# Performance work log

Hardware: AMD Instinct MI355X
Metric: run time of the kernel (lower is better)

## Reference

```python
import jax, jax.numpy as jnp
import numpy as np


def setup_inputs() -> dict:
    key = jax.random.key(0)
    ks = jax.random.split(key, 6)
    b, t, s, qu, vu, d = 8, 64, 512, 512, 512, 512
    return {
        "query": jax.random.normal(ks[0], (b, t, qu), jnp.float32),
        "value": jax.random.normal(ks[1], (b, s, vu), jnp.float32),
        "mask": jax.random.randint(ks[2], (b, s), 0, 2).astype(bool),
        "W1_w": jax.random.normal(ks[3], (qu, d), jnp.float32) * (1.0 / np.sqrt(qu)),
        "W1_b": jnp.zeros((d,), jnp.float32),
        "W2_w": jax.random.normal(ks[4], (vu, d), jnp.float32) * (1.0 / np.sqrt(vu)),
        "W2_b": jnp.zeros((d,), jnp.float32),
        "scale": jax.random.normal(ks[5], (d,), jnp.float32) * 0.05,
    }


def reference(query, value, mask, W1_w, W1_b, W2_w, W2_b, scale):
    # Dense projections
    q = jnp.einsum('btq,qd->btd', query, W1_w) + W1_b   # [b,t,d]
    k = jnp.einsum('bsv,vd->bsd', value, W2_w) + W2_b   # [b,s,d]
    # Additive (Bahdanau) score with learned scale vector (Keras use_scale=True)
    # scores[b,t,s] = sum_d scale[d] * tanh(q[b,t,d] + k[b,s,d])
    scores = jnp.einsum('btsd,d->bts', jnp.tanh(q[:, :, None, :] + k[:, None, :, :]), scale)
    # Mask over source positions (value mask); query mask is all-ones (no-op)
    scores = jnp.where(mask[:, None, :], scores, jnp.float32(-1e9))
    attention_weights = jax.nn.softmax(scores, axis=-1)   # [b,t,s]
    context_vector = jnp.einsum('bts,bsv->btv', attention_weights, value)  # [b,t,vu]
    return context_vector, attention_weights
```

## Files before the change

kernel.cpp:

```cpp
#include <hip/hip_runtime.h>
#include <hip/hip_bf16.h>

#define B_  8
#define T_  64
#define S_  512
#define D_  512

#define QN (512 * 512)
#define KN (4096 * 512)
#define SN (B_ * T_ * S_)

#define TLOG2E 2.8853900817779268f
#define LOG2E  1.4426950408889634f

typedef __attribute__((ext_vector_type(8))) short bf16x8;
typedef __attribute__((ext_vector_type(4))) float f32x4;

__device__ __forceinline__ unsigned short f2bf(float f) {
    unsigned int u = __float_as_uint(f);
    return (unsigned short)((u + 0x7FFFu + ((u >> 16) & 1u)) >> 16);
}
__device__ __forceinline__ unsigned int pk2(float a, float b) {
    return (unsigned int)f2bf(a) | ((unsigned int)f2bf(b) << 16);
}

__global__ __launch_bounds__(256) void mfma_gemm(
    const float* __restrict__ query, const float* __restrict__ value,
    const float* __restrict__ W1, const float* __restrict__ W2,
    const float* __restrict__ b1, const float* __restrict__ b2,
    float* __restrict__ qproj, float* __restrict__ kproj)
{
    __shared__ __align__(16) unsigned short Ab[64][40];
    __shared__ __align__(16) unsigned short Bs[64][40];

    const int x = blockIdx.x;
    const float *A, *W;
    float* C;
    int tm, tn;
    bool isq;
    if (x < 512) {
        tm = (x & 7) * 8 + ((x >> 3) & 7);
        tn = x >> 6;
        A = value; W = W2; C = kproj; isq = false;
    } else {
        int r = x - 512;
        tm = r >> 3; tn = r & 7;
        A = query; W = W1; C = qproj; isq = true;
    }

    const int tid  = threadIdx.x;
    const int lane = tid & 63;
    const int wid  = tid >> 6;
    const int wm = (wid & 1) * 32, wn = (wid >> 1) * 32;
    const int fm = lane & 15, fq = lane >> 4;

    f32x4 acc00 = {0.f, 0.f, 0.f, 0.f};
    f32x4 acc01 = acc00, acc10 = acc00, acc11 = acc00;

    const int ar = tid >> 2;
    const int ac = (tid & 3) * 8;
    const float* Ag = A + (size_t)(tm * 64 + ar) * 512 + ac;
    const int c0 = (tid & 15) * 4;
    const int kp = (tid >> 4) * 2;
    const float* Wg = W + (size_t)kp * 512 + tn * 64 + c0;

    float4 av0 = *(const float4*)(Ag);
    float4 av1 = *(const float4*)(Ag + 4);
    float4 wv0 = *(const float4*)(Wg);
    float4 wv1 = *(const float4*)(Wg + 512);

    for (int k0 = 0; k0 < 512; k0 += 32) {
        __syncthreads();
        {
            uint4 pa;
            pa.x = pk2(av0.x, av0.y); pa.y = pk2(av0.z, av0.w);
            pa.z = pk2(av1.x, av1.y); pa.w = pk2(av1.z, av1.w);
            *(uint4*)&Ab[ar][ac] = pa;
            *(unsigned int*)&Bs[c0 + 0][kp] = pk2(wv0.x, wv1.x);
            *(unsigned int*)&Bs[c0 + 1][kp] = pk2(wv0.y, wv1.y);
            *(unsigned int*)&Bs[c0 + 2][kp] = pk2(wv0.z, wv1.z);
            *(unsigned int*)&Bs[c0 + 3][kp] = pk2(wv0.w, wv1.w);
        }
        __syncthreads();
        const int kn = (k0 + 32) & 511;
        av0 = *(const float4*)(Ag + kn);
        av1 = *(const float4*)(Ag + kn + 4);
        wv0 = *(const float4*)(Wg + (size_t)kn * 512);
        wv1 = *(const float4*)(Wg + (size_t)kn * 512 + 512);

        bf16x8 a0  = *(const bf16x8*)&Ab[wm + fm][fq * 8];
        bf16x8 a1  = *(const bf16x8*)&Ab[wm + 16 + fm][fq * 8];
        bf16x8 b0  = *(const bf16x8*)&Bs[wn + fm][fq * 8];
        bf16x8 b1v = *(const bf16x8*)&Bs[wn + 16 + fm][fq * 8];
        acc00 = __builtin_amdgcn_mfma_f32_16x16x32_bf16(a0, b0,  acc00, 0, 0, 0);
        acc01 = __builtin_amdgcn_mfma_f32_16x16x32_bf16(a0, b1v, acc01, 0, 0, 0);
        acc10 = __builtin_amdgcn_mfma_f32_16x16x32_bf16(a1, b0,  acc10, 0, 0, 0);
        acc11 = __builtin_amdgcn_mfma_f32_16x16x32_bf16(a1, b1v, acc11, 0, 0, 0);
    }

    const int n0 = tn * 64 + wn + fm;
    const int n1 = n0 + 16;
    float bias0 = 0.f, bias1 = 0.f;
    if (isq) {
        bias0 = b1[n0] + b2[n0];
        bias1 = b1[n1] + b2[n1];
    }
    const int m0 = tm * 64 + wm + fq * 4;
#pragma unroll
    for (int r = 0; r < 4; ++r) {
        C[(size_t)(m0 + r) * 512 + n0]      = (acc00[r] + bias0) * TLOG2E;
        C[(size_t)(m0 + r) * 512 + n1]      = (acc01[r] + bias1) * TLOG2E;
        C[(size_t)(m0 + 16 + r) * 512 + n0] = (acc10[r] + bias0) * TLOG2E;
        C[(size_t)(m0 + 16 + r) * 512 + n1] = (acc11[r] + bias1) * TLOG2E;
    }
}

__global__ __launch_bounds__(256, 4) void scores_t(
    const float* __restrict__ qproj, const float* __restrict__ kproj,
    const int*   __restrict__ mask,  const float* __restrict__ scale,
    float* __restrict__ sparts)
{
    const int blk = blockIdx.x;
    const int b  = blk & 7;
    int r = blk >> 3;
    const int dh = r & 1;
    r >>= 1;
    const int sg = r & 31;
    const int tg = r >> 5;
    const int t0 = tg * 16, s0 = sg * 16;
    const int dbase = dh * 256;

    __shared__ float kT[16][132];
    __shared__ float qT[16][132];
    __shared__ float cS[128];

    const int tid  = threadIdx.x;
    const int t_l = tid >> 4;
    const int s_l = tid & 15;
    const int m = mask[b * S_ + s0 + s_l];

    const int lrow = tid >> 5;
    const int lcol = (tid & 31) * 4;

    float p0 = 0.f, p1 = 0.f;

    for (int c = 0; c < 2; ++c) {
        const int dc = dbase + c * 128;
        const float* kp = kproj + (size_t)(b * S_ + s0) * D_ + dc;
        const float* qp = qproj + (size_t)(b * T_ + t0) * D_ + dc;
        *(float4*)&kT[lrow][lcol]     = *(const float4*)(kp + (size_t)lrow * D_ + lcol);
        *(float4*)&kT[lrow + 8][lcol] = *(const float4*)(kp + (size_t)(lrow + 8) * D_ + lcol);
        *(float4*)&qT[lrow][lcol]     = *(const float4*)(qp + (size_t)lrow * D_ + lcol);
        *(float4*)&qT[lrow + 8][lcol] = *(const float4*)(qp + (size_t)(lrow + 8) * D_ + lcol);
        if (tid < 32) {
            *(float4*)&cS[tid * 4] = *(const float4*)(scale + dc + tid * 4);
        }
        __syncthreads();

#pragma unroll 4
        for (int j = 0; j < 32; ++j) {
            float4 k4 = *(const float4*)&kT[s_l][j * 4];
            float4 q4 = *(const float4*)&qT[t_l][j * 4];
            float4 c4 = *(const float4*)&cS[j * 4];
            float e0 = __builtin_amdgcn_exp2f(q4.x + k4.x);
            float e1 = __builtin_amdgcn_exp2f(q4.y + k4.y);
            float e2 = __builtin_amdgcn_exp2f(q4.z + k4.z);
            float e3 = __builtin_amdgcn_exp2f(q4.w + k4.w);
            float r0 = __builtin_amdgcn_rcpf(e0 + 1.0f);
            float r1 = __builtin_amdgcn_rcpf(e1 + 1.0f);
            float r2 = __builtin_amdgcn_rcpf(e2 + 1.0f);
            float r3 = __builtin_amdgcn_rcpf(e3 + 1.0f);
            p0 = fmaf(c4.x, r0, p0);
            p1 = fmaf(c4.y, r1, p1);
            p0 = fmaf(c4.z, r2, p0);
            p1 = fmaf(c4.w, r3, p1);
        }
        __syncthreads();
    }

    const float p = p0 + p1;
    const float out = m ? (-2.0f * p) : -5e8f;
    sparts[(size_t)dh * SN + (size_t)(b * T_ + t0 + t_l) * S_ + s0 + s_l] = out;
}

__global__ __launch_bounds__(256) void softmax_ctx(
    const float* __restrict__ sparts, const float* __restrict__ value,
    float* __restrict__ ctx, float* __restrict__ attn)
{
    const int blk = blockIdx.x;
    const int b = blk & 7;
    int r = blk >> 3;
    const int vc = r & 3;
    const int tq = r >> 2;
    const int t0 = tq * 4;
    const size_t rbase = (size_t)(b * T_ + t0) * S_;

    const int tid  = threadIdx.x;
    const int lane = tid & 63;
    const int wid  = tid >> 6;

    __shared__ float4 wp4[S_];
    __shared__ float4 part[4][8][32];
    __shared__ float4 red4[8];

    const int sa = tid, sb = tid + 256;
    float4 xa, xb;
    xa.x = sparts[rbase + sa]          + sparts[SN + rbase + sa];
    xa.y = sparts[rbase + S_ + sa]     + sparts[SN + rbase + S_ + sa];
    xa.z = sparts[rbase + 2 * S_ + sa] + sparts[SN + rbase + 2 * S_ + sa];
    xa.w = sparts[rbase + 3 * S_ + sa] + sparts[SN + rbase + 3 * S_ + sa];
    xb.x = sparts[rbase + sb]          + sparts[SN + rbase + sb];
    xb.y = sparts[rbase + S_ + sb]     + sparts[SN + rbase + S_ + sb];
    xb.z = sparts[rbase + 2 * S_ + sb] + sparts[SN + rbase + 2 * S_ + sb];
    xb.w = sparts[rbase + 3 * S_ + sb] + sparts[SN + rbase + 3 * S_ + sb];

    float4 m4;
    m4.x = fmaxf(xa.x, xb.x); m4.y = fmaxf(xa.y, xb.y);
    m4.z = fmaxf(xa.z, xb.z); m4.w = fmaxf(xa.w, xb.w);
#pragma unroll
    for (int off = 32; off >= 1; off >>= 1) {
        m4.x = fmaxf(m4.x, __shfl_xor(m4.x, off));
        m4.y = fmaxf(m4.y, __shfl_xor(m4.y, off));
        m4.z = fmaxf(m4.z, __shfl_xor(m4.z, off));
        m4.w = fmaxf(m4.w, __shfl_xor(m4.w, off));
    }
    if (lane == 0) red4[wid] = m4;
    __syncthreads();
    {
        float4 r0 = red4[0], r1 = red4[1], r2 = red4[2], r3 = red4[3];
        m4.x = fmaxf(fmaxf(r0.x, r1.x), fmaxf(r2.x, r3.x));
        m4.y = fmaxf(fmaxf(r0.y, r1.y), fmaxf(r2.y, r3.y));
        m4.z = fmaxf(fmaxf(r0.z, r1.z), fmaxf(r2.z, r3.z));
        m4.w = fmaxf(fmaxf(r0.w, r1.w), fmaxf(r2.w, r3.w));
    }

    float4 ea, eb;
    ea.x = __builtin_amdgcn_exp2f((xa.x - m4.x) * LOG2E);
    ea.y = __builtin_amdgcn_exp2f((xa.y - m4.y) * LOG2E);
    ea.z = __builtin_amdgcn_exp2f((xa.z - m4.z) * LOG2E);
    ea.w = __builtin_amdgcn_exp2f((xa.w - m4.w) * LOG2E);
    eb.x = __builtin_amdgcn_exp2f((xb.x - m4.x) * LOG2E);
    eb.y = __builtin_amdgcn_exp2f((xb.y - m4.y) * LOG2E);
    eb.z = __builtin_amdgcn_exp2f((xb.z - m4.z) * LOG2E);
    eb.w = __builtin_amdgcn_exp2f((xb.w - m4.w) * LOG2E);

    float4 s4;
    s4.x = ea.x + eb.x; s4.y = ea.y + eb.y;
    s4.z = ea.z + eb.z; s4.w = ea.w + eb.w;
#pragma unroll
    for (int off = 32; off >= 1; off >>= 1) {
        s4.x += __shfl_xor(s4.x, off);
        s4.y += __shfl_xor(s4.y, off);
        s4.z += __shfl_xor(s4.z, off);
        s4.w += __shfl_xor(s4.w, off);
    }
    if (lane == 0) red4[4 + wid] = s4;
    __syncthreads();
    {
        float4 r0 = red4[4], r1 = red4[5], r2 = red4[6], r3 = red4[7];
        s4.x = (r0.x + r1.x) + (r2.x + r3.x);
        s4.y = (r0.y + r1.y) + (r2.y + r3.y);
        s4.z = (r0.z + r1.z) + (r2.z + r3.z);
        s4.w = (r0.w + r1.w) + (r2.w + r3.w);
    }
    float4 inv4;
    inv4.x = 1.0f / s4.x; inv4.y = 1.0f / s4.y;
    inv4.z = 1.0f / s4.z; inv4.w = 1.0f / s4.w;

    float4 wa, wb;
    wa.x = ea.x * inv4.x; wa.y = ea.y * inv4.y;
    wa.z = ea.z * inv4.z; wa.w = ea.w * inv4.w;
    wb.x = eb.x * inv4.x; wb.y = eb.y * inv4.y;
    wb.z = eb.z * inv4.z; wb.w = eb.w * inv4.w;

    wp4[sa] = wa;
    wp4[sb] = wb;
    if (vc == 0) {
        attn[rbase + sa]          = wa.x; attn[rbase + sb]          = wb.x;
        attn[rbase + S_ + sa]     = wa.y; attn[rbase + S_ + sb]     = wb.y;
        attn[rbase + 2 * S_ + sa] = wa.z; attn[rbase + 2 * S_ + sb] = wb.z;
        attn[rbase + 3 * S_ + sa] = wa.w; attn[rbase + 3 * S_ + sb] = wb.w;
    }
    __syncthreads();

    const int ssub = wid * 2 + (lane >> 5);
    const int v4   = lane & 31;
    const int v    = vc * 128 + v4 * 4;
    const float* vb = value + ((size_t)(b * S_) + ssub * 64) * D_ + v;
    float4 a0; a0.x = 0.f; a0.y = 0.f; a0.z = 0.f; a0.w = 0.f;
    float4 a1 = a0, a2 = a0, a3 = a0;
#pragma unroll 4
    for (int i = 0; i < 64; ++i) {
        float4 vv = *(const float4*)(vb + (size_t)i * D_);
        float4 w4 = wp4[ssub * 64 + i];
        a0.x = fmaf(w4.x, vv.x, a0.x); a0.y = fmaf(w4.x, vv.y, a0.y);
        a0.z = fmaf(w4.x, vv.z, a0.z); a0.w = fmaf(w4.x, vv.w, a0.w);
        a1.x = fmaf(w4.y, vv.x, a1.x); a1.y = fmaf(w4.y, vv.y, a1.y);
        a1.z = fmaf(w4.y, vv.z, a1.z); a1.w = fmaf(w4.y, vv.w, a1.w);
        a2.x = fmaf(w4.z, vv.x, a2.x); a2.y = fmaf(w4.z, vv.y, a2.y);
        a2.z = fmaf(w4.z, vv.z, a2.z); a2.w = fmaf(w4.z, vv.w, a2.w);
        a3.x = fmaf(w4.w, vv.x, a3.x); a3.y = fmaf(w4.w, vv.y, a3.y);
        a3.z = fmaf(w4.w, vv.z, a3.z); a3.w = fmaf(w4.w, vv.w, a3.w);
    }
    part[0][ssub][v4] = a0;
    part[1][ssub][v4] = a1;
    part[2][ssub][v4] = a2;
    part[3][ssub][v4] = a3;
    __syncthreads();
    if (tid < 128) {
        const int ts = tid >> 5, w4i = tid & 31;
        float4 p0 = part[ts][0][w4i], p1 = part[ts][1][w4i];
        float4 p2 = part[ts][2][w4i], p3 = part[ts][3][w4i];
        float4 p4 = part[ts][4][w4i], p5 = part[ts][5][w4i];
        float4 p6 = part[ts][6][w4i], p7 = part[ts][7][w4i];
        float4 o;
        o.x = ((p0.x + p1.x) + (p2.x + p3.x)) + ((p4.x + p5.x) + (p6.x + p7.x));
        o.y = ((p0.y + p1.y) + (p2.y + p3.y)) + ((p4.y + p5.y) + (p6.y + p7.y));
        o.z = ((p0.z + p1.z) + (p2.z + p3.z)) + ((p4.z + p5.z) + (p6.z + p7.z));
        o.w = ((p0.w + p1.w) + (p2.w + p3.w)) + ((p4.w + p5.w) + (p6.w + p7.w));
        *(float4*)(ctx + (size_t)(b * T_ + t0 + ts) * D_ + vc * 128 + w4i * 4) = o;
    }
}

extern "C" void kernel_launch(void* const* d_in, const int* in_sizes, int n_in,
                              void* d_out, int out_size, void* d_ws, size_t ws_size,
                              hipStream_t stream) {
    const float* query = (const float*)d_in[0];
    const float* value = (const float*)d_in[1];
    const int*   mask  = (const int*)  d_in[2];
    const float* W1w   = (const float*)d_in[3];
    const float* W1b   = (const float*)d_in[4];
    const float* W2w   = (const float*)d_in[5];
    const float* W2b   = (const float*)d_in[6];
    const float* scale = (const float*)d_in[7];

    float* ctx  = (float*)d_out;
    float* attn = (float*)d_out + (size_t)B_ * T_ * D_;

    float* qproj = (float*)d_ws;
    float* kproj = qproj + (size_t)QN;
    float* spart = kproj + (size_t)KN;

    mfma_gemm<<<576, 256, 0, stream>>>(query, value, W1w, W2w, W1b, W2b,
                                       qproj, kproj);
    scores_t<<<2048, 256, 0, stream>>>(qproj, kproj, mask, scale, spart);
    softmax_ctx<<<512, 256, 0, stream>>>(spart, value, ctx, attn);
}
```

Before: 131.8 us.

## Fuse score computation with softmax and context into one kernel per query pair

Merges the scores and softmax/context kernels into a single fused_attn kernel in which each block handles two query rows of one batch, with one thread per source position. The second row's exp is derived from the first through a precomputed per-d factor exp2(q1-q0), so it costs an extra rcp but no extra exp. This removes the intermediate score buffer and one launch. It also reduces the grid to 256 blocks of 512 threads, which may leave the chip underfilled. Each thread streams a full kproj row from global memory instead of from shared tiles, and exp2(q1-q0) can overflow for large differences.

```diff
diff --git a/kernel.cpp b/kernel.cpp
--- a/kernel.cpp
+++ b/kernel.cpp
@@ -8,7 +8,6 @@
 
 #define QN (512 * 512)
 #define KN (4096 * 512)
-#define SN (B_ * T_ * S_)
 
 #define TLOG2E 2.8853900817779268f
 #define LOG2E  1.4426950408889634f
@@ -16,12 +15,10 @@
 typedef __attribute__((ext_vector_type(8))) short bf16x8;
 typedef __attribute__((ext_vector_type(4))) float f32x4;
 
-__device__ __forceinline__ unsigned short f2bf(float f) {
-    unsigned int u = __float_as_uint(f);
-    return (unsigned short)((u + 0x7FFFu + ((u >> 16) & 1u)) >> 16);
-}
 __device__ __forceinline__ unsigned int pk2(float a, float b) {
-    return (unsigned int)f2bf(a) | ((unsigned int)f2bf(b) << 16);
+    float2 f; f.x = a; f.y = b;
+    __hip_bfloat162 h = __float22bfloat162_rn(f);
+    return *(unsigned int*)&h;
 }
 
 __global__ __launch_bounds__(256) void mfma_gemm(
@@ -115,210 +112,156 @@
     }
 }
 
-__global__ __launch_bounds__(256, 4) void scores_t(
+__global__ __launch_bounds__(512, 2) void fused_attn(
     const float* __restrict__ qproj, const float* __restrict__ kproj,
     const int*   __restrict__ mask,  const float* __restrict__ scale,
-    float* __restrict__ sparts)
+    const float* __restrict__ value,
+    float* __restrict__ ctx, float* __restrict__ attn)
 {
     const int blk = blockIdx.x;
     const int b  = blk & 7;
-    int r = blk >> 3;
-    const int dh = r & 1;
-    r >>= 1;
-    const int sg = r & 31;
-    const int tg = r >> 5;
-    const int t0 = tg * 16, s0 = sg * 16;
-    const int dbase = dh * 256;
-
-    __shared__ float kT[16][132];
-    __shared__ float qT[16][132];
-    __shared__ float cS[128];
-
-    const int tid  = threadIdx.x;
-    const int t_l = tid >> 4;
-    const int s_l = tid & 15;
-    const int m = mask[b * S_ + s0 + s_l];
-
-    const int lrow = tid >> 5;
-    const int lcol = (tid & 31) * 4;
-
-    float p0 = 0.f, p1 = 0.f;
-
-    for (int c = 0; c < 2; ++c) {
-        const int dc = dbase + c * 128;
-        const float* kp = kproj + (size_t)(b * S_ + s0) * D_ + dc;
-        const float* qp = qproj + (size_t)(b * T_ + t0) * D_ + dc;
-        *(float4*)&kT[lrow][lcol]     = *(const float4*)(kp + (size_t)lrow * D_ + lcol);
-        *(float4*)&kT[lrow + 8][lcol] = *(const float4*)(kp + (size_t)(lrow + 8) * D_ + lcol);
-        *(float4*)&qT[lrow][lcol]     = *(const float4*)(qp + (size_t)lrow * D_ + lcol);
-        *(float4*)&qT[lrow + 8][lcol] = *(const float4*)(qp + (size_t)(lrow + 8) * D_ + lcol);
-        if (tid < 32) {
-            *(float4*)&cS[tid * 4] = *(const float4*)(scale + dc + tid * 4);
-        }
-        __syncthreads();
-
-#pragma unroll 4
-        for (int j = 0; j < 32; ++j) {
-            float4 k4 = *(const float4*)&kT[s_l][j * 4];
-            float4 q4 = *(const float4*)&qT[t_l][j * 4];
-            float4 c4 = *(const float4*)&cS[j * 4];
-            float e0 = __builtin_amdgcn_exp2f(q4.x + k4.x);
-            float e1 = __builtin_amdgcn_exp2f(q4.y + k4.y);
-            float e2 = __builtin_amdgcn_exp2f(q4.z + k4.z);
-            float e3 = __builtin_amdgcn_exp2f(q4.w + k4.w);
-            float r0 = __builtin_amdgcn_rcpf(e0 + 1.0f);
-            float r1 = __builtin_amdgcn_rcpf(e1 + 1.0f);
-            float r2 = __builtin_amdgcn_rcpf(e2 + 1.0f);
-            float r3 = __builtin_amdgcn_rcpf(e3 + 1.0f);
-            p0 = fmaf(c4.x, r0, p0);
-            p1 = fmaf(c4.y, r1, p1);
-            p0 = fmaf(c4.z, r2, p0);
-            p1 = fmaf(c4.w, r3, p1);
-        }
-        __syncthreads();
-    }
-
-    const float p = p0 + p1;
-    const float out = m ? (-2.0f * p) : -5e8f;
-    sparts[(size_t)dh * SN + (size_t)(b * T_ + t0 + t_l) * S_ + s0 + s_l] = out;
-}
-
-__global__ __launch_bounds__(256) void softmax_ctx(
-    const float* __restrict__ sparts, const float* __restrict__ value,
-    float* __restrict__ ctx, float* __restrict__ attn)
-{
-    const int blk = blockIdx.x;
-    const int b = blk & 7;
-    int r = blk >> 3;
-    const int vc = r & 3;
-    const int tq = r >> 2;
-    const int t0 = tq * 4;
-    const size_t rbase = (size_t)(b * T_ + t0) * S_;
+    const int tp = blk >> 3;
+    const size_t row0 = (size_t)(b * T_ + tp * 2);
+
+    __shared__ __align__(16) float q0A[512];
+    __shared__ __align__(16) float dA[512];
+    __shared__ __align__(16) float cA[512];
+    __shared__ __align__(16) float2 wp2[512];
+    __shared__ __align__(16) float4 part[2][4][128];
+    __shared__ float2 red2[16];
 
     const int tid  = threadIdx.x;
     const int lane = tid & 63;
     const int wid  = tid >> 6;
 
-    __shared__ float4 wp4[S_];
-    __shared__ float4 part[4][8][32];
-    __shared__ float4 red4[8];
-
-    const int sa = tid, sb = tid + 256;
-    float4 xa, xb;
-    xa.x = sparts[rbase + sa]          + sparts[SN + rbase + sa];
-    xa.y = sparts[rbase + S_ + sa]     + sparts[SN + rbase + S_ + sa];
-    xa.z = sparts[rbase + 2 * S_ + sa] + sparts[SN + rbase + 2 * S_ + sa];
-    xa.w = sparts[rbase + 3 * S_ + sa] + sparts[SN + rbase + 3 * S_ + sa];
-    xb.x = sparts[rbase + sb]          + sparts[SN + rbase + sb];
-    xb.y = sparts[rbase + S_ + sb]     + sparts[SN + rbase + S_ + sb];
-    xb.z = sparts[rbase + 2 * S_ + sb] + sparts[SN + rbase + 2 * S_ + sb];
-    xb.w = sparts[rbase + 3 * S_ + sb] + sparts[SN + rbase + 3 * S_ + sb];
-
-    float4 m4;
-    m4.x = fmaxf(xa.x, xb.x); m4.y = fmaxf(xa.y, xb.y);
-    m4.z = fmaxf(xa.z, xb.z); m4.w = fmaxf(xa.w, xb.w);
+    {
+        float q0v = qproj[row0 * D_ + tid];
+        float q1v = qproj[(row0 + 1) * D_ + tid];
+        q0A[tid] = q0v;
+        dA[tid]  = __builtin_amdgcn_exp2f(q1v - q0v);
+        cA[tid]  = scale[tid];
+    }
+    __syncthreads();
+
+    const int s = tid;
+    const int m = mask[b * S_ + s];
+    const float* kr = kproj + (size_t)(b * S_ + s) * D_;
+    float p0 = 0.f, p1 = 0.f;
+
+    float4 kf0 = ((const float4*)kr)[0];
+    float4 kf1 = ((const float4*)kr)[1];
+    float4 kf2 = ((const float4*)kr)[2];
+    float4 kf3 = ((const float4*)kr)[3];
+
+#define SC_STEP(K4, DD) do {                                                  \
+        float4 q4 = *(const float4*)&q0A[DD];                                 \
+        float4 dl = *(const float4*)&dA[DD];                                  \
+        float4 c4 = *(const float4*)&cA[DD];                                  \
+        float e, ra, rb;                                                      \
+        e  = __builtin_amdgcn_exp2f(q4.x + (K4).x);                           \
+        ra = __builtin_amdgcn_rcpf(e + 1.0f);                                 \
+        rb = __builtin_amdgcn_rcpf(fmaf(e, dl.x, 1.0f));                      \
+        p0 = fmaf(c4.x, ra, p0); p1 = fmaf(c4.x, rb, p1);                     \
+        e  = __builtin_amdgcn_exp2f(q4.y + (K4).y);                           \
+        ra = __builtin_amdgcn_rcpf(e + 1.0f);                                 \
+        rb = __builtin_amdgcn_rcpf(fmaf(e, dl.y, 1.0f));                      \
+        p0 = fmaf(c4.y, ra, p0); p1 = fmaf(c4.y, rb, p1);                     \
+        e  = __builtin_amdgcn_exp2f(q4.z + (K4).z);                           \
+        ra = __builtin_amdgcn_rcpf(e + 1.0f);                                 \
+        rb = __builtin_amdgcn_rcpf(fmaf(e, dl.z, 1.0f));                      \
+        p0 = fmaf(c4.z, ra, p0); p1 = fmaf(c4.z, rb, p1);                     \
+        e  = __builtin_amdgcn_exp2f(q4.w + (K4).w);                           \
+        ra = __builtin_amdgcn_rcpf(e + 1.0f);                                 \
+        rb = __builtin_amdgcn_rcpf(fmaf(e, dl.w, 1.0f));                      \
+        p0 = fmaf(c4.w, ra, p0); p1 = fmaf(c4.w, rb, p1);                     \
+    } while (0)
+
+    for (int c = 0; c < 32; ++c) {
+        const int nx = ((c + 1) & 31) * 16;
+        float4 nf0 = ((const float4*)(kr + nx))[0];
+        float4 nf1 = ((const float4*)(kr + nx))[1];
+        float4 nf2 = ((const float4*)(kr + nx))[2];
+        float4 nf3 = ((const float4*)(kr + nx))[3];
+        const int d0 = c * 16;
+        SC_STEP(kf0, d0);
+        SC_STEP(kf1, d0 + 4);
+        SC_STEP(kf2, d0 + 8);
+        SC_STEP(kf3, d0 + 12);
+        kf0 = nf0; kf1 = nf1; kf2 = nf2; kf3 = nf3;
+    }
+#undef SC_STEP
+
+    float x0 = m ? (-2.0f * p0) : -1e9f;
+    float x1 = m ? (-2.0f * p1) : -1e9f;
+
+    float2 mx; mx.x = x0; mx.y = x1;
 #pragma unroll
     for (int off = 32; off >= 1; off >>= 1) {
-        m4.x = fmaxf(m4.x, __shfl_xor(m4.x, off));
-        m4.y = fmaxf(m4.y, __shfl_xor(m4.y, off));
-        m4.z = fmaxf(m4.z, __shfl_xor(m4.z, off));
-        m4.w = fmaxf(m4.w, __shfl_xor(m4.w, off));
-    }
-    if (lane == 0) red4[wid] = m4;
-    __syncthreads();
-    {
-        float4 r0 = red4[0], r1 = red4[1], r2 = red4[2], r3 = red4[3];
-        m4.x = fmaxf(fmaxf(r0.x, r1.x), fmaxf(r2.x, r3.x));
-        m4.y = fmaxf(fmaxf(r0.y, r1.y), fmaxf(r2.y, r3.y));
-        m4.z = fmaxf(fmaxf(r0.z, r1.z), fmaxf(r2.z, r3.z));
-        m4.w = fmaxf(fmaxf(r0.w, r1.w), fmaxf(r2.w, r3.w));
-    }
-
-    float4 ea, eb;
-    ea.x = __builtin_amdgcn_exp2f((xa.x - m4.x) * LOG2E);
-    ea.y = __builtin_amdgcn_exp2f((xa.y - m4.y) * LOG2E);
-    ea.z = __builtin_amdgcn_exp2f((xa.z - m4.z) * LOG2E);
-    ea.w = __builtin_amdgcn_exp2f((xa.w - m4.w) * LOG2E);
-    eb.x = __builtin_amdgcn_exp2f((xb.x - m4.x) * LOG2E);
-    eb.y = __builtin_amdgcn_exp2f((xb.y - m4.y) * LOG2E);
-    eb.z = __builtin_amdgcn_exp2f((xb.z - m4.z) * LOG2E);
-    eb.w = __builtin_amdgcn_exp2f((xb.w - m4.w) * LOG2E);
-
-    float4 s4;
-    s4.x = ea.x + eb.x; s4.y = ea.y + eb.y;
-    s4.z = ea.z + eb.z; s4.w = ea.w + eb.w;
+        mx.x = fmaxf(mx.x, __shfl_xor(mx.x, off));
+        mx.y = fmaxf(mx.y, __shfl_xor(mx.y, off));
+    }
+    if (lane == 0) red2[wid] = mx;
+    __syncthreads();
+    float2 M = red2[0];
+#pragma unroll
+    for (int i = 1; i < 8; ++i) {
+        M.x = fmaxf(M.x, red2[i].x);
+        M.y = fmaxf(M.y, red2[i].y);
+    }
+
+    float e0 = __builtin_amdgcn_exp2f((x0 - M.x) * LOG2E);
+    float e1 = __builtin_amdgcn_exp2f((x1 - M.y) * LOG2E);
+    float2 sm; sm.x = e0; sm.y = e1;
 #pragma unroll
     for (int off = 32; off >= 1; off >>= 1) {
-        s4.x += __shfl_xor(s4.x, off);
-        s4.y += __shfl_xor(s4.y, off);
-        s4.z += __shfl_xor(s4.z, off);
-        s4.w += __shfl_xor(s4.w, off);
-    }
-    if (lane == 0) red4[4 + wid] = s4;
-    __syncthreads();
-    {
-        float4 r0 = red4[4], r1 = red4[5], r2 = red4[6], r3 = red4[7];
-        s4.x = (r0.x + r1.x) + (r2.x + r3.x);
-        s4.y = (r0.y + r1.y) + (r2.y + r3.y);
-        s4.z = (r0.z + r1.z) + (r2.z + r3.z);
-        s4.w = (r0.w + r1.w) + (r2.w + r3.w);
-    }
-    float4 inv4;
-    inv4.x = 1.0f / s4.x; inv4.y = 1.0f / s4.y;
-    inv4.z = 1.0f / s4.z; inv4.w = 1.0f / s4.w;
-
-    float4 wa, wb;
-    wa.x = ea.x * inv4.x; wa.y = ea.y * inv4.y;
-    wa.z = ea.z * inv4.z; wa.w = ea.w * inv4.w;
-    wb.x = eb.x * inv4.x; wb.y = eb.y * inv4.y;
-    wb.z = eb.z * inv4.z; wb.w = eb.w * inv4.w;
-
-    wp4[sa] = wa;
-    wp4[sb] = wb;
-    if (vc == 0) {
-        attn[rbase + sa]          = wa.x; attn[rbase + sb]          = wb.x;
-        attn[rbase + S_ + sa]     = wa.y; attn[rbase + S_ + sb]     = wb.y;
-        attn[rbase + 2 * S_ + sa] = wa.z; attn[rbase + 2 * S_ + sb] = wb.z;
-        attn[rbase + 3 * S_ + sa] = wa.w; attn[rbase + 3 * S_ + sb] = wb.w;
-    }
-    __syncthreads();
-
-    const int ssub = wid * 2 + (lane >> 5);
-    const int v4   = lane & 31;
-    const int v    = vc * 128 + v4 * 4;
-    const float* vb = value + ((size_t)(b * S_) + ssub * 64) * D_ + v;
+        sm.x += __shfl_xor(sm.x, off);
+        sm.y += __shfl_xor(sm.y, off);
+    }
+    if (lane == 0) red2[8 + wid] = sm;
+    __syncthreads();
+    float2 SS = red2[8];
+#pragma unroll
+    for (int i = 9; i < 16; ++i) {
+        SS.x += red2[i].x;
+        SS.y += red2[i].y;
+    }
+    const float inv0 = __builtin_amdgcn_rcpf(SS.x);
+    const float inv1 = __builtin_amdgcn_rcpf(SS.y);
+    const float w0 = e0 * inv0, w1 = e1 * inv1;
+
+    float2 wpair; wpair.x = w0; wpair.y = w1;
+    wp2[s] = wpair;
+    attn[row0 * S_ + s]       = w0;
+    attn[(row0 + 1) * S_ + s] = w1;
+    __syncthreads();
+
+    const int g  = tid >> 7;
+    const int v4 = tid & 127;
+    const float* vb = value + ((size_t)(b * S_) + g * 128) * D_ + v4 * 4;
     float4 a0; a0.x = 0.f; a0.y = 0.f; a0.z = 0.f; a0.w = 0.f;
-    float4 a1 = a0, a2 = a0, a3 = a0;
+    float4 a1 = a0;
 #pragma unroll 4
-    for (int i = 0; i < 64; ++i) {
+    for (int i = 0; i < 128; ++i) {
         float4 vv = *(const float4*)(vb + (size_t)i * D_);
-        float4 w4 = wp4[ssub * 64 + i];
-        a0.x = fmaf(w4.x, vv.x, a0.x); a0.y = fmaf(w4.x, vv.y, a0.y);
-        a0.z = fmaf(w4.x, vv.z, a0.z); a0.w = fmaf(w4.x, vv.w, a0.w);
-        a1.x = fmaf(w4.y, vv.x, a1.x); a1.y = fmaf(w4.y, vv.y, a1.y);
-        a1.z = fmaf(w4.y, vv.z, a1.z); a1.w = fmaf(w4.y, vv.w, a1.w);
-        a2.x = fmaf(w4.z, vv.x, a2.x); a2.y = fmaf(w4.z, vv.y, a2.y);
-        a2.z = fmaf(w4.z, vv.z, a2.z); a2.w = fmaf(w4.z, vv.w, a2.w);
-        a3.x = fmaf(w4.w, vv.x, a3.x); a3.y = fmaf(w4.w, vv.y, a3.y);
-        a3.z = fmaf(w4.w, vv.z, a3.z); a3.w = fmaf(w4.w, vv.w, a3.w);
-    }
-    part[0][ssub][v4] = a0;
-    part[1][ssub][v4] = a1;
-    part[2][ssub][v4] = a2;
-    part[3][ssub][v4] = a3;
-    __syncthreads();
-    if (tid < 128) {
-        const int ts = tid >> 5, w4i = tid & 31;
-        float4 p0 = part[ts][0][w4i], p1 = part[ts][1][w4i];
-        float4 p2 = part[ts][2][w4i], p3 = part[ts][3][w4i];
-        float4 p4 = part[ts][4][w4i], p5 = part[ts][5][w4i];
-        float4 p6 = part[ts][6][w4i], p7 = part[ts][7][w4i];
+        float2 w = wp2[g * 128 + i];
+        a0.x = fmaf(w.x, vv.x, a0.x); a0.y = fmaf(w.x, vv.y, a0.y);
+        a0.z = fmaf(w.x, vv.z, a0.z); a0.w = fmaf(w.x, vv.w, a0.w);
+        a1.x = fmaf(w.y, vv.x, a1.x); a1.y = fmaf(w.y, vv.y, a1.y);
+        a1.z = fmaf(w.y, vv.z, a1.z); a1.w = fmaf(w.y, vv.w, a1.w);
+    }
+    part[0][g][v4] = a0;
+    part[1][g][v4] = a1;
+    __syncthreads();
+    if (tid < 256) {
+        const int t = tid >> 7, v = tid & 127;
+        float4 p0v = part[t][0][v], p1v = part[t][1][v];
+        float4 p2v = part[t][2][v], p3v = part[t][3][v];
         float4 o;
-        o.x = ((p0.x + p1.x) + (p2.x + p3.x)) + ((p4.x + p5.x) + (p6.x + p7.x));
-        o.y = ((p0.y + p1.y) + (p2.y + p3.y)) + ((p4.y + p5.y) + (p6.y + p7.y));
-        o.z = ((p0.z + p1.z) + (p2.z + p3.z)) + ((p4.z + p5.z) + (p6.z + p7.z));
-        o.w = ((p0.w + p1.w) + (p2.w + p3.w)) + ((p4.w + p5.w) + (p6.w + p7.w));
-        *(float4*)(ctx + (size_t)(b * T_ + t0 + ts) * D_ + vc * 128 + w4i * 4) = o;
+        o.x = (p0v.x + p1v.x) + (p2v.x + p3v.x);
+        o.y = (p0v.y + p1v.y) + (p2v.y + p3v.y);
+        o.z = (p0v.z + p1v.z) + (p2v.z + p3v.z);
+        o.w = (p0v.w + p1v.w) + (p2v.w + p3v.w);
+        *(float4*)(ctx + (row0 + t) * D_ + v * 4) = o;
     }
 }
 
@@ -339,10 +282,9 @@
 
     float* qproj = (float*)d_ws;
     float* kproj = qproj + (size_t)QN;
-    float* spart = kproj + (size_t)KN;
 
     mfma_gemm<<<576, 256, 0, stream>>>(query, value, W1w, W2w, W1b, W2b,
                                        qproj, kproj);
-    scores_t<<<2048, 256, 0, stream>>>(qproj, kproj, mask, scale, spart);
-    softmax_ctx<<<512, 256, 0, stream>>>(spart, value, ctx, attn);
-}
+    fused_attn<<<256, 512, 0, stream>>>(qproj, kproj, mask, scale, value,
+                                        ctx, attn);
+}
```

After: 136.3 us. 3.4% more time.
